# Performance work log

Hardware: AMD Instinct MI355X
Metric: run time of the kernel (lower is better)

Reference implementation:

```python
import jax, jax.numpy as jnp
import numpy as np

B, S, D, H, F = 8, 1024, 1024, 16, 4096
DH = D // H  # 64
EPS = 1e-12


def _layer_norm(x, g, b):
    mu = jnp.mean(x, axis=-1, keepdims=True)
    var = jnp.mean(jnp.square(x - mu), axis=-1, keepdims=True)
    return (x - mu) / jnp.sqrt(var + EPS) * g + b


def setup_inputs() -> dict:
    key = jax.random.key(0)
    ks = jax.random.split(key, 16)
    sd = 0.02
    inp = {
        "x": jax.random.normal(ks[0], (B, S, D), dtype=jnp.float32),
        "attn_mask": jnp.ones((B, S), dtype=jnp.int32),
        # attention projections (torch Linear: W is [out, in])
        "Wq": jax.random.normal(ks[1], (D, D), dtype=jnp.float32) * sd,
        "bq": jnp.zeros((D,), dtype=jnp.float32),
        "Wk": jax.random.normal(ks[2], (D, D), dtype=jnp.float32) * sd,
        "bk": jnp.zeros((D,), dtype=jnp.float32),
        "Wv": jax.random.normal(ks[3], (D, D), dtype=jnp.float32) * sd,
        "bv": jnp.zeros((D,), dtype=jnp.float32),
        "Wo": jax.random.normal(ks[4], (D, D), dtype=jnp.float32) * sd,
        "bo": jnp.zeros((D,), dtype=jnp.float32),
        # sa_layer_norm
        "ln1_g": jnp.ones((D,), dtype=jnp.float32),
        "ln1_b": jnp.zeros((D,), dtype=jnp.float32),
        # FFN
        "W1": jax.random.normal(ks[5], (F, D), dtype=jnp.float32) * sd,
        "b1": jnp.zeros((F,), dtype=jnp.float32),
        "W2": jax.random.normal(ks[6], (D, F), dtype=jnp.float32) * sd,
        "b2": jnp.zeros((D,), dtype=jnp.float32),
        # output_layer_norm
        "ln2_g": jnp.ones((D,), dtype=jnp.float32),
        "ln2_b": jnp.zeros((D,), dtype=jnp.float32),
    }
    return inp


def reference(x, attn_mask, Wq, bq, Wk, bk, Wv, bv, Wo, bo,
              ln1_g, ln1_b, W1, b1, W2, b2, ln2_g, ln2_b):
    b, s, d = x.shape

    def proj_heads(inp, W, bias):
        y = jnp.einsum('bsd,ed->bse', inp, W) + bias  # torch Linear: x @ W.T + b
        return y.reshape(b, s, H, DH).transpose(0, 2, 1, 3)  # (b, h, s, dh)

    q = proj_heads(x, Wq, bq) / jnp.sqrt(jnp.float32(DH))
    k = proj_heads(x, Wk, bk)
    v = proj_heads(x, Wv, bv)

    scores = jnp.einsum('bhqe,bhke->bhqk', q, k)  # (b, h, s, s)
    pad = (attn_mask == 0)[:, None, None, :]      # (b, 1, 1, s)
    scores = jnp.where(pad, -jnp.inf, scores)
    weights = jax.nn.softmax(scores, axis=-1)

    ctx = jnp.einsum('bhqk,bhke->bhqe', weights, v)
    ctx = ctx.transpose(0, 2, 1, 3).reshape(b, s, d)
    sa_out = jnp.einsum('bsd,ed->bse', ctx, Wo) + bo

    h = _layer_norm(sa_out + x, ln1_g, ln1_b)

    ff = jnp.einsum('bsd,fd->bsf', h, W1) + b1
    ff = jax.nn.gelu(ff, approximate=False)
    ff = jnp.einsum('bsf,df->bsd', ff, W2) + b2

    out = _layer_norm(ff + h, ln2_g, ln2_b)
    return out
```

## Files before the change

### kernel.cpp

```cpp
#include <hip/hip_runtime.h>
#include <math.h>

typedef __attribute__((ext_vector_type(8))) short short8;
typedef __attribute__((ext_vector_type(4))) float f32x4;

__device__ __forceinline__ unsigned short f2bf(float f) {
  unsigned int u = __float_as_uint(f);
  u += 0x7fffu + ((u >> 16) & 1u);
  return (unsigned short)(u >> 16);
}

__device__ __forceinline__ float gelu_f(float v) {
  float xa = fabsf(v) * 0.70710678118f;
  float t = __builtin_amdgcn_rcpf(1.f + 0.3275911f * xa);
  float p = t * (0.254829592f +
            t * (-0.284496736f +
            t * (1.421413741f +
            t * (-1.453152027f + t * 1.061405429f))));
  float erfa = 1.f - p * __expf(-xa * xa);
  return 0.5f * v * (1.f + copysignf(erfa, v));
}

__device__ __forceinline__ void gll16(const unsigned short* g, unsigned short* l) {
  __builtin_amdgcn_global_load_lds(
      (const __attribute__((address_space(1))) unsigned int*)(uintptr_t)g,
      (__attribute__((address_space(3))) unsigned int*)(uintptr_t)l, 16, 0, 0);
}

__global__ __launch_bounds__(256) void cvt_all(
    const float* __restrict__ Wq, const float* __restrict__ Wk,
    const float* __restrict__ Wv, const float* __restrict__ Wo,
    const float* __restrict__ W1, const float* __restrict__ W2,
    const float* __restrict__ x, unsigned short* __restrict__ ws) {
  const int bi = blockIdx.x;
  const float* in;
  unsigned short* out;
  int i;
  if (bi < 4096) {
    const int m = bi >> 10;
    in = (m == 0) ? Wq : (m == 1) ? Wk : (m == 2) ? Wv : Wo;
    out = ws + (size_t)m * (1u << 20);
    i = (bi & 1023) * 256 + threadIdx.x;
  } else if (bi < 8192) {
    in = W1; out = ws + (4u << 20); i = (bi - 4096) * 256 + threadIdx.x;
  } else if (bi < 12288) {
    in = W2; out = ws + (8u << 20); i = (bi - 8192) * 256 + threadIdx.x;
  } else {
    in = x; out = ws + (12u << 20); i = (bi - 12288) * 256 + threadIdx.x;
  }
  float4 f = reinterpret_cast<const float4*>(in)[i];
  ushort4 o;
  o.x = f2bf(f.x); o.y = f2bf(f.y); o.z = f2bf(f.z); o.w = f2bf(f.w);
  reinterpret_cast<ushort4*>(out)[i] = o;
}

template <int EPI, bool SWAP>
__global__ __launch_bounds__(256) void gemm_nt(
    const unsigned short* __restrict__ A, const unsigned short* __restrict__ B,
    const float* __restrict__ bias, const float* __restrict__ bias_k,
    int K, int N, const float* __restrict__ resid,
    unsigned short* __restrict__ outb, float* __restrict__ outf) {
  __shared__ __align__(16) unsigned short As[2][128 * 32];
  __shared__ __align__(16) unsigned short Bs[2][128 * 32];
  const int t = threadIdx.x;
  const int tm = blockIdx.y * 128, tn = blockIdx.x * 128;
  const int lane = t & 63, wv = t >> 6;
  const int wr = wv >> 1, wc = wv & 1;
  const int l15 = lane & 15, quad = lane >> 4;
  const int srow = lane >> 2;
  const int scol = (lane & 3) << 3;

  const unsigned short* pa0 = &A[(size_t)(tm + wv * 32 + srow) * K + scol];
  const unsigned short* pa1 = &A[(size_t)(tm + wv * 32 + 16 + srow) * K + scol];
  const unsigned short* pb0 = &B[(size_t)(tn + wv * 32 + srow) * K + scol];
  const unsigned short* pb1 = &B[(size_t)(tn + wv * 32 + 16 + srow) * K + scol];
  unsigned short* la0 = &As[0][(wv * 2) * 512];
  unsigned short* la1 = &As[0][(wv * 2 + 1) * 512];
  unsigned short* lb0 = &Bs[0][(wv * 2) * 512];
  unsigned short* lb1 = &Bs[0][(wv * 2 + 1) * 512];

  const f32x4 zero = {0.f, 0.f, 0.f, 0.f};
  f32x4 acc[4][4];
#pragma unroll
  for (int i = 0; i < 4; ++i)
#pragma unroll
    for (int j = 0; j < 4; ++j) acc[i][j] = zero;

  gll16(pa0, la0); pa0 += 32;
  gll16(pa1, la1); pa1 += 32;
  gll16(pb0, lb0); pb0 += 32;
  gll16(pb1, lb1); pb1 += 32;

  const int nIter = K >> 5;
  for (int it = 0; it < nIter; ++it) {
    __syncthreads();
    const int cur = (it & 1) * 4096;
    const int nxt = 4096 - cur;
    if (it + 1 < nIter) {
      gll16(pa0, la0 + nxt); pa0 += 32;
      gll16(pa1, la1 + nxt); pa1 += 32;
      gll16(pb0, lb0 + nxt); pb0 += 32;
      gll16(pb1, lb1 + nxt); pb1 += 32;
    }
    short8 af[4], bfr[4];
#pragma unroll
    for (int i = 0; i < 4; ++i) {
      af[i] = *reinterpret_cast<const short8*>(&As[0][cur + (wr * 64 + i * 16 + l15) * 32 + quad * 8]);
      bfr[i] = *reinterpret_cast<const short8*>(&Bs[0][cur + (wc * 64 + i * 16 + l15) * 32 + quad * 8]);
    }
#pragma unroll
    for (int i = 0; i < 4; ++i)
#pragma unroll
      for (int j = 0; j < 4; ++j)
        acc[i][j] = SWAP
            ? __builtin_amdgcn_mfma_f32_16x16x32_bf16(bfr[j], af[i], acc[i][j], 0, 0, 0)
            : __builtin_amdgcn_mfma_f32_16x16x32_bf16(af[i], bfr[j], acc[i][j], 0, 0, 0);
  }

  if (SWAP) {
#pragma unroll
    for (int i = 0; i < 4; ++i) {
      const int row = tm + wr * 64 + i * 16 + l15;
#pragma unroll
      for (int j = 0; j < 4; ++j) {
        const int col0 = tn + wc * 64 + j * 16 + quad * 4;
        if (EPI == 2) {
          const float4 b4 = *reinterpret_cast<const float4*>(&bias[col0]);
          ushort4 pk;
          pk.x = f2bf(gelu_f(acc[i][j][0] + b4.x));
          pk.y = f2bf(gelu_f(acc[i][j][1] + b4.y));
          pk.z = f2bf(gelu_f(acc[i][j][2] + b4.z));
          pk.w = f2bf(gelu_f(acc[i][j][3] + b4.w));
          *reinterpret_cast<ushort4*>(&outb[(size_t)row * (size_t)N + col0]) = pk;
        } else {
          const float4 b4 = *reinterpret_cast<const float4*>(&bias[col0]);
          const size_t idx = (size_t)row * (size_t)N + col0;
          const float4 r4 = *reinterpret_cast<const float4*>(&resid[idx]);
          float4 o4;
          o4.x = acc[i][j][0] + b4.x + r4.x;
          o4.y = acc[i][j][1] + b4.y + r4.y;
          o4.z = acc[i][j][2] + b4.z + r4.z;
          o4.w = acc[i][j][3] + b4.w + r4.w;
          *reinterpret_cast<float4*>(&outf[idx]) = o4;
        }
      }
    }
  } else {
#pragma unroll
    for (int i = 0; i < 4; ++i) {
#pragma unroll
      for (int j = 0; j < 4; ++j) {
        const int col = tn + wc * 64 + j * 16 + l15;
        const float bcol = bias[col];
        const int h = col >> 6, dh = col & 63;
        const int row0 = tm + wr * 64 + i * 16 + quad * 4;
        const int b = row0 >> 10, s0 = row0 & 1023;
        ushort4 pk;
        pk.x = f2bf(acc[i][j][0] + bcol);
        pk.y = f2bf(acc[i][j][1] + bcol);
        pk.z = f2bf(acc[i][j][2] + bcol);
        pk.w = f2bf(acc[i][j][3] + bcol);
        *reinterpret_cast<ushort4*>(
            &outb[(((size_t)((b << 4) + h)) << 16) + (dh << 10) + s0]) = pk;
      }
    }
  }
}

#define MFMA_Q(mh, nh)                                                        \
  {                                                                           \
    __builtin_amdgcn_s_setprio(1);                                            \
    _Pragma("unroll") for (int i = 0; i < 4; ++i) {                           \
      _Pragma("unroll") for (int jj = 0; jj < NREP / 2; ++jj) {               \
        const int j = (nh) * (NREP / 2) + jj;                                 \
        acc[(mh) * 4 + i][j] = __builtin_amdgcn_mfma_f32_16x16x32_bf16(       \
            bf[j][0], af[i][0], acc[(mh) * 4 + i][j], 0, 0, 0);               \
        acc[(mh) * 4 + i][j] = __builtin_amdgcn_mfma_f32_16x16x32_bf16(       \
            bf[j][1], af[i][1], acc[(mh) * 4 + i][j], 0, 0, 0);               \
      }                                                                       \
    }                                                                         \
    __builtin_amdgcn_s_setprio(0);                                            \
  }

#define READ_A(mh)                                                            \
  _Pragma("unroll") for (int i = 0; i < 4; ++i) {                             \
    af[i][0] = *reinterpret_cast<const short8*>(                              \
        &Asc[abase + ((mh) * 64 + i * 16) * 64 + s0]);                        \
    af[i][1] = *reinterpret_cast<const short8*>(                              \
        &Asc[abase + ((mh) * 64 + i * 16) * 64 + s1]);                        \
  }

#define LGKM0                                                                 \
  asm volatile("s_waitcnt lgkmcnt(0)" ::: "memory");                          \
  __builtin_amdgcn_sched_barrier(0)

#define MEMFENCE asm volatile("" ::: "memory")

template <int EPI, int BN>
__global__ __launch_bounds__(512, 2) void gemm_big(
    const unsigned short* __restrict__ A, const unsigned short* __restrict__ B,
    const float* __restrict__ bias, const float* __restrict__ bias_k,
    int K, int N, const float* __restrict__ resid,
    unsigned short* __restrict__ outb, float* __restrict__ outf) {
  constexpr int WN = BN / 4;
  constexpr int NREP = WN / 16;
  constexpr int BGRP = BN / 64;
  __shared__ __align__(16) unsigned short As[2][256 * 64];
  __shared__ __align__(16) unsigned short Bs[2][BN * 64];

  const int t = threadIdx.x;
  const int lane = t & 63, wv = t >> 6;
  const int wm = wv >> 2, wn = wv & 3;
  const int l15 = lane & 15, quad = lane >> 4;

  const int gx = gridDim.x;
  const int nwg = gx * gridDim.y;
  int lin = blockIdx.y * gx + blockIdx.x;
  lin = (lin & 7) * (nwg >> 3) + (lin >> 3);
  const int gxs = 31 - __clz(gx);
  const int tn = (lin & (gx - 1)) * BN;
  const int tm = (lin >> gxs) * 256;

  const int srow = lane >> 3;
  const int scol = ((lane & 7) ^ srow) << 3;
  const unsigned short* pA[4];
  const unsigned short* pB[BGRP];
#pragma unroll
  for (int g = 0; g < 4; ++g)
    pA[g] = &A[(size_t)(tm + g * 64 + wv * 8 + srow) * K + scol];
#pragma unroll
  for (int g = 0; g < BGRP; ++g)
    pB[g] = &B[(size_t)(tn + g * 64 + wv * 8 + srow) * K + scol];

  const int abase = (wm * 128 + l15) * 64;
  const int bbase = (wn * WN + l15) * 64;
  const int s0 = ((quad ^ (l15 & 7)) << 3);
  const int s1 = (((quad + 4) ^ (l15 & 7)) << 3);

  const f32x4 zero = {0.f, 0.f, 0.f, 0.f};
  f32x4 acc[8][NREP];
#pragma unroll
  for (int i = 0; i < 8; ++i)
#pragma unroll
    for (int j = 0; j < NREP; ++j) acc[i][j] = zero;
  short8 af[4][2], bf[NREP][2];

#pragma unroll
  for (int g = 0; g < 4; ++g) gll16(pA[g], &As[0][(g * 64 + wv * 8) * 64]);
#pragma unroll
  for (int g = 0; g < BGRP; ++g) gll16(pB[g], &Bs[0][(g * 64 + wv * 8) * 64]);
#pragma unroll
  for (int g = 0; g < 4; ++g) {
    pA[g] += 64;
    gll16(pA[g], &As[1][(g * 64 + wv * 8) * 64]);
    pA[g] += 64;
  }
#pragma unroll
  for (int g = 0; g < BGRP; ++g) {
    pB[g] += 64;
    gll16(pB[g], &Bs[1][(g * 64 + wv * 8) * 64]);
    pB[g] += 64;
  }
  if constexpr (BGRP == 4) asm volatile("s_waitcnt vmcnt(8)" ::: "memory");
  else asm volatile("s_waitcnt vmcnt(6)" ::: "memory");
  __builtin_amdgcn_s_barrier();
  MEMFENCE;

  const int NT = K >> 6;
  for (int tt = 0; tt < NT; ++tt) {
    const unsigned short* Asc = As[tt & 1];
    const unsigned short* Bsc = Bs[tt & 1];
    unsigned short* Asw = As[tt & 1];
    unsigned short* Bsw = Bs[tt & 1];
    const bool st = (tt + 2 < NT);

    READ_A(0);
#pragma unroll
    for (int j = 0; j < NREP; ++j) {
      bf[j][0] = *reinterpret_cast<const short8*>(&Bsc[bbase + (j * 16) * 64 + s0]);
      bf[j][1] = *reinterpret_cast<const short8*>(&Bsc[bbase + (j * 16) * 64 + s1]);
    }
    LGKM0;
    MFMA_Q(0, 0);
    MFMA_Q(0, 1);
    __builtin_amdgcn_s_barrier();
    MEMFENCE;
    if (st) {
      gll16(pA[0], &Asw[(0 * 64 + wv * 8) * 64]);
      gll16(pA[2], &Asw[(2 * 64 + wv * 8) * 64]);
      gll16(pB[0], &Bsw[(0 * 64 + wv * 8) * 64]);
      if constexpr (BGRP == 4) gll16(pB[1], &Bsw[(1 * 64 + wv * 8) * 64]);
    }
    READ_A(1);
    LGKM0;
    MFMA_Q(1, 0);
    __builtin_amdgcn_s_barrier();
    MEMFENCE;
    if (st) {
      gll16(pA[1], &Asw[(1 * 64 + wv * 8) * 64]);
      gll16(pA[3], &Asw[(3 * 64 + wv * 8) * 64]);
      if constexpr (BGRP == 4) {
        gll16(pB[2], &Bsw[(2 * 64 + wv * 8) * 64]);
        gll16(pB[3], &Bsw[(3 * 64 + wv * 8) * 64]);
      } else {
        gll16(pB[1], &Bsw[(1 * 64 + wv * 8) * 64]);
      }
#pragma unroll
      for (int g = 0; g < 4; ++g) pA[g] += 64;
#pragma unroll
      for (int g = 0; g < BGRP; ++g) pB[g] += 64;
    }
    MFMA_Q(1, 1);
    if (st) {
      if constexpr (BGRP == 4) asm volatile("s_waitcnt vmcnt(8)" ::: "memory");
      else asm volatile("s_waitcnt vmcnt(6)" ::: "memory");
    } else {
      asm volatile("s_waitcnt vmcnt(0)" ::: "memory");
    }
    __builtin_amdgcn_s_barrier();
    MEMFENCE;
  }

  const int rb = tm + wm * 128 + l15;
  const int cb = tn + wn * WN + (quad << 2);
#pragma unroll
  for (int i = 0; i < 8; ++i) {
    const int row = rb + i * 16;
#pragma unroll
    for (int j = 0; j < NREP; ++j) {
      const int col0 = cb + j * 16;
      if constexpr (EPI == 5) {
        const int chunk = col0 >> 10;
        const int colc = col0 & 1023;
        const float4 b4 = *reinterpret_cast<const float4*>(
            &(chunk == 0 ? bias : bias_k)[colc]);
        const float sc = (chunk == 0) ? 0.125f : 1.f;
        const int h = colc >> 6, dh = colc & 63;
        const int b = row >> 10, s = row & 1023;
        ushort4 pk;
        pk.x = f2bf((acc[i][j][0] + b4.x) * sc);
        pk.y = f2bf((acc[i][j][1] + b4.y) * sc);
        pk.z = f2bf((acc[i][j][2] + b4.z) * sc);
        pk.w = f2bf((acc[i][j][3] + b4.w) * sc);
        *reinterpret_cast<ushort4*>(
            &outb[((size_t)chunk << 23) + (((size_t)((b << 4) + h)) << 16) +
                  (s << 6) + dh]) = pk;
      } else if constexpr (EPI == 2) {
        const float4 b4 = *reinterpret_cast<const float4*>(&bias[col0]);
        ushort4 pk;
        pk.x = f2bf(gelu_f(acc[i][j][0] + b4.x));
        pk.y = f2bf(gelu_f(acc[i][j][1] + b4.y));
        pk.z = f2bf(gelu_f(acc[i][j][2] + b4.z));
        pk.w = f2bf(gelu_f(acc[i][j][3] + b4.w));
        *reinterpret_cast<ushort4*>(&outb[(size_t)row * (size_t)N + col0]) = pk;
      } else {
        const float4 b4 = *reinterpret_cast<const float4*>(&bias[col0]);
        const size_t idx = (size_t)row * (size_t)N + col0;
        const float4 r4 = *reinterpret_cast<const float4*>(&resid[idx]);
        float4 o4;
        o4.x = acc[i][j][0] + b4.x + r4.x;
        o4.y = acc[i][j][1] + b4.y + r4.y;
        o4.z = acc[i][j][2] + b4.z + r4.z;
        o4.w = acc[i][j][3] + b4.w + r4.w;
        *reinterpret_cast<float4*>(&outf[idx]) = o4;
      }
    }
  }
}
#undef MFMA_Q
#undef READ_A
#undef LGKM0
#undef MEMFENCE

__global__ __launch_bounds__(256) void attn_kernel(
    const unsigned short* __restrict__ Q, const unsigned short* __restrict__ Kc,
    const unsigned short* __restrict__ Vg, const int* __restrict__ mask,
    unsigned short* __restrict__ ctx) {
  __shared__ __align__(16) unsigned short Ks[2][64 * 64];
  __shared__ __align__(16) unsigned short Vs[2][64 * 64];
  __shared__ __align__(16) unsigned short Ps[4][16 * 72];
  __shared__ float maskf[1024];
  const int t = threadIdx.x;
  const int bh = blockIdx.x;
  const int qt = blockIdx.y;
  const int b = bh >> 4, h = bh & 15;
  const int lane = t & 63, wv = t >> 6, l15 = lane & 15, quad = lane >> 4;
  const int lr = lane >> 3;
  const int cs = (lane & 7) ^ lr;
  const unsigned short* Qp = Q + ((size_t)bh << 16);
  const unsigned short* Kp = Kc + ((size_t)bh << 16);
  const unsigned short* Vp = Vg + ((size_t)bh << 16);
  const int seg0 = wv * 2, seg1 = wv * 2 + 1;
  const int r0 = seg0 * 8 + lr, r1 = seg1 * 8 + lr;

  for (int i = t; i < 1024; i += 256)
    maskf[i] = mask[b * 1024 + i] ? -8.f : -INFINITY;

  short8 qf[2][2];
#pragma unroll
  for (int g = 0; g < 2; ++g)
#pragma unroll
    for (int hh = 0; hh < 2; ++hh)
      qf[g][hh] = *reinterpret_cast<const short8*>(
          &Qp[(size_t)(qt * 128 + wv * 32 + g * 16 + l15) * 64 + hh * 32 + quad * 8]);

  gll16(&Kp[r0 * 64 + cs * 8], &Ks[0][seg0 * 512]);
  gll16(&Kp[r1 * 64 + cs * 8], &Ks[0][seg1 * 512]);
  gll16(&Vp[r0 * 1024 + cs * 8], &Vs[0][seg0 * 512]);
  gll16(&Vp[r1 * 1024 + cs * 8], &Vs[0][seg1 * 512]);

  const int sw0 = ((quad ^ (l15 & 7)) << 3);
  const int sw1 = (((quad + 4) ^ (l15 & 7)) << 3);
  const f32x4 zero = {0.f, 0.f, 0.f, 0.f};
  float ps[2][4];
  f32x4 o[2][4];
#pragma unroll
  for (int g = 0; g < 2; ++g)
#pragma unroll
    for (int j = 0; j < 4; ++j) { o[g][j] = zero; ps[g][j] = 0.f; }

  unsigned short* Pw = Ps[wv];
  for (int kt = 0; kt < 16; ++kt) {
    __syncthreads();
    const int cur = kt & 1;
    if (kt < 15) {
      const int nb = cur ^ 1;
      gll16(&Kp[((kt + 1) * 64 + r0) * 64 + cs * 8], &Ks[nb][seg0 * 512]);
      gll16(&Kp[((kt + 1) * 64 + r1) * 64 + cs * 8], &Ks[nb][seg1 * 512]);
      gll16(&Vp[r0 * 1024 + (kt + 1) * 64 + cs * 8], &Vs[nb][seg0 * 512]);
      gll16(&Vp[r1 * 1024 + (kt + 1) * 64 + cs * 8], &Vs[nb][seg1 * 512]);
    }
    float madd[4];
    short8 kf[4][2];
#pragma unroll
    for (int nt = 0; nt < 4; ++nt) {
      const int row = (nt * 16 + l15) * 64;
      kf[nt][0] = *reinterpret_cast<const short8*>(&Ks[cur][row + sw0]);
      kf[nt][1] = *reinterpret_cast<const short8*>(&Ks[cur][row + sw1]);
      madd[nt] = maskf[kt * 64 + nt * 16 + l15];
    }
#pragma unroll
    for (int g = 0; g < 2; ++g) {
      f32x4 s4[4];
#pragma unroll
      for (int nt = 0; nt < 4; ++nt) {
        s4[nt] = __builtin_amdgcn_mfma_f32_16x16x32_bf16(qf[g][0], kf[nt][0], zero, 0, 0, 0);
        s4[nt] = __builtin_amdgcn_mfma_f32_16x16x32_bf16(qf[g][1], kf[nt][1], s4[nt], 0, 0, 0);
      }
#pragma unroll
      for (int nt = 0; nt < 4; ++nt) {
#pragma unroll
        for (int r = 0; r < 4; ++r) {
          float p = __expf(s4[nt][r] + madd[nt]);
          ps[g][r] += p;
          Pw[(quad * 4 + r) * 72 + nt * 16 + l15] = f2bf(p);
        }
      }
      short8 pf0 = *reinterpret_cast<const short8*>(&Pw[l15 * 72 + quad * 8]);
      short8 pf1 = *reinterpret_cast<const short8*>(&Pw[l15 * 72 + 32 + quad * 8]);
#pragma unroll
      for (int nt = 0; nt < 4; ++nt) {
        const int row = (nt * 16 + l15) * 64;
        short8 vf0 = *reinterpret_cast<const short8*>(&Vs[cur][row + sw0]);
        short8 vf1 = *reinterpret_cast<const short8*>(&Vs[cur][row + sw1]);
        o[g][nt] = __builtin_amdgcn_mfma_f32_16x16x32_bf16(pf0, vf0, o[g][nt], 0, 0, 0);
        o[g][nt] = __builtin_amdgcn_mfma_f32_16x16x32_bf16(pf1, vf1, o[g][nt], 0, 0, 0);
      }
    }
  }

#pragma unroll
  for (int g = 0; g < 2; ++g)
#pragma unroll
    for (int r = 0; r < 4; ++r) {
      float v = ps[g][r];
#pragma unroll
      for (int off = 8; off >= 1; off >>= 1) v += __shfl_xor(v, off, 64);
      const float inv = 1.f / v;
      const int srow = qt * 128 + wv * 32 + g * 16 + quad * 4 + r;
#pragma unroll
      for (int nt = 0; nt < 4; ++nt) {
        const int dh = nt * 16 + l15;
        ctx[((size_t)b << 20) + ((size_t)srow << 10) + (h << 6) + dh] =
            f2bf(o[g][nt][r] * inv);
      }
    }
}

__global__ __launch_bounds__(256) void ln_kernel(float* __restrict__ y,
                                                 const float* __restrict__ g,
                                                 const float* __restrict__ be,
                                                 unsigned short* __restrict__ hb) {
  __shared__ float sm[8];
  const int t = threadIdx.x;
  const size_t row = blockIdx.x;
  float* yr = y + (row << 10);
  float v[4];
#pragma unroll
  for (int i = 0; i < 4; ++i) v[i] = yr[t + (i << 8)];
  float s = v[0] + v[1] + v[2] + v[3];
#pragma unroll
  for (int off = 32; off >= 1; off >>= 1) s += __shfl_xor(s, off, 64);
  if ((t & 63) == 0) sm[t >> 6] = s;
  __syncthreads();
  float mu = (sm[0] + sm[1] + sm[2] + sm[3]) * (1.f / 1024.f);
  float q = 0.f;
#pragma unroll
  for (int i = 0; i < 4; ++i) { float d = v[i] - mu; q += d * d; }
#pragma unroll
  for (int off = 32; off >= 1; off >>= 1) q += __shfl_xor(q, off, 64);
  if ((t & 63) == 0) sm[4 + (t >> 6)] = q;
  __syncthreads();
  float var = (sm[4] + sm[5] + sm[6] + sm[7]) * (1.f / 1024.f);
  float rs = rsqrtf(var + 1e-12f);
#pragma unroll
  for (int i = 0; i < 4; ++i) {
    int c = t + (i << 8);
    float o = (v[i] - mu) * rs * g[c] + be[c];
    yr[c] = o;
    if (hb) hb[(row << 10) + c] = f2bf(o);
  }
}

extern "C" void kernel_launch(void* const* d_in, const int* in_sizes, int n_in,
                              void* d_out, int out_size, void* d_ws, size_t ws_size,
                              hipStream_t stream) {
  const float* x   = (const float*)d_in[0];
  const int*   msk = (const int*)d_in[1];
  const float* Wq  = (const float*)d_in[2];
  const float* bq  = (const float*)d_in[3];
  const float* Wk  = (const float*)d_in[4];
  const float* bk  = (const float*)d_in[5];
  const float* Wv  = (const float*)d_in[6];
  const float* bv  = (const float*)d_in[7];
  const float* Wo  = (const float*)d_in[8];
  const float* bo  = (const float*)d_in[9];
  const float* g1  = (const float*)d_in[10];
  const float* be1 = (const float*)d_in[11];
  const float* W1  = (const float*)d_in[12];
  const float* b1  = (const float*)d_in[13];
  const float* W2  = (const float*)d_in[14];
  const float* b2  = (const float*)d_in[15];
  const float* g2  = (const float*)d_in[16];
  const float* be2 = (const float*)d_in[17];
  float* out = (float*)d_out;

  unsigned short* Wqb = (unsigned short*)d_ws;
  unsigned short* Wvb = Wqb + (2u << 20);
  unsigned short* Wob = Wvb + (1u << 20);
  unsigned short* W1b = Wob + (1u << 20);
  unsigned short* W2b = W1b + (4u << 20);
  unsigned short* xb  = W2b + (4u << 20);
  unsigned short* qb  = xb + (8u << 20);
  unsigned short* vb  = qb + (16u << 20);
  unsigned short* ctx = xb;
  unsigned short* ffb = xb;
  float* y1 = (float*)(qb + (24u << 20));
  unsigned short* hb = (unsigned short*)(y1 + (8u << 20));

  dim3 blk(256), blk5(512);
  cvt_all<<<dim3(20480), blk, 0, stream>>>(Wq, Wk, Wv, Wo, W1, W2, x, (unsigned short*)d_ws);
  gemm_big<5, 256><<<dim3(8, 32), blk5, 0, stream>>>(xb, Wqb, bq, bk, 1024, 2048,
                                                     nullptr, qb, nullptr);
  gemm_nt<4, false><<<dim3(8, 64), blk, 0, stream>>>(xb, Wvb, bv, nullptr, 1024, 1024,
                                                     nullptr, vb, nullptr);
  attn_kernel<<<dim3(128, 8), blk, 0, stream>>>(qb, qb + (8u << 20), vb, msk, ctx);
  gemm_big<1, 128><<<dim3(8, 32), blk5, 0, stream>>>(ctx, Wob, bo, nullptr, 1024, 1024,
                                                     x, nullptr, y1);
  ln_kernel<<<dim3(8192), blk, 0, stream>>>(y1, g1, be1, hb);
  gemm_big<2, 256><<<dim3(16, 32), blk5, 0, stream>>>(hb, W1b, b1, nullptr, 1024, 4096,
                                                      nullptr, ffb, nullptr);
  gemm_big<1, 128><<<dim3(8, 32), blk5, 0, stream>>>(ffb, W2b, b2, nullptr, 4096, 1024,
                                                     y1, nullptr, out);
  ln_kernel<<<dim3(8192), blk, 0, stream>>>(out, g2, be2, nullptr);
}
```

Baseline: 501.5 us.

## Unify V projection into gemm_big and restructure its LDS/MFMA interleave schedule

Removes the older 128x128 gemm_nt kernel and routes the V projection through gemm_big with a new SWAP template flag that handles the transposed V output layout. The main loop of gemm_big is reorganised into four quarter phases, each with its own LDS read, barrier, MFMA block and staggered global-to-LDS prefetch. The aim is to overlap LDS fragment reads and global loads more finely with MFMA work. It adds more barriers per iteration, which could cost extra synchronisation.

```diff
diff --git a/kernel.cpp b/kernel.cpp
--- a/kernel.cpp
+++ b/kernel.cpp
@@ -54,77 +54,229 @@
   reinterpret_cast<ushort4*>(out)[i] = o;
 }
 
-template <int EPI, bool SWAP>
-__global__ __launch_bounds__(256) void gemm_nt(
+#define MFMA_Q(mh, nh)                                                        \
+  {                                                                           \
+    __builtin_amdgcn_s_setprio(1);                                            \
+    _Pragma("unroll") for (int i = 0; i < 4; ++i) {                           \
+      _Pragma("unroll") for (int jj = 0; jj < NREP / 2; ++jj) {               \
+        const int j = (nh) * (NREP / 2) + jj;                                 \
+        if constexpr (SWAP) {                                                 \
+          acc[(mh) * 4 + i][j] = __builtin_amdgcn_mfma_f32_16x16x32_bf16(     \
+              bf[j][0], af[i][0], acc[(mh) * 4 + i][j], 0, 0, 0);             \
+          acc[(mh) * 4 + i][j] = __builtin_amdgcn_mfma_f32_16x16x32_bf16(     \
+              bf[j][1], af[i][1], acc[(mh) * 4 + i][j], 0, 0, 0);             \
+        } else {                                                              \
+          acc[(mh) * 4 + i][j] = __builtin_amdgcn_mfma_f32_16x16x32_bf16(     \
+              af[i][0], bf[j][0], acc[(mh) * 4 + i][j], 0, 0, 0);             \
+          acc[(mh) * 4 + i][j] = __builtin_amdgcn_mfma_f32_16x16x32_bf16(     \
+              af[i][1], bf[j][1], acc[(mh) * 4 + i][j], 0, 0, 0);             \
+        }                                                                     \
+      }                                                                       \
+    }                                                                         \
+    __builtin_amdgcn_s_setprio(0);                                            \
+  }
+
+#define READ_A(mh)                                                            \
+  _Pragma("unroll") for (int i = 0; i < 4; ++i) {                             \
+    af[i][0] = *reinterpret_cast<const short8*>(                              \
+        &Asc[abase + ((mh) * 64 + i * 16) * 64 + s0]);                        \
+    af[i][1] = *reinterpret_cast<const short8*>(                              \
+        &Asc[abase + ((mh) * 64 + i * 16) * 64 + s1]);                        \
+  }
+
+#define READ_B(nh)                                                            \
+  _Pragma("unroll") for (int jj = 0; jj < NREP / 2; ++jj) {                   \
+    const int j = (nh) * (NREP / 2) + jj;                                     \
+    bf[j][0] = *reinterpret_cast<const short8*>(                              \
+        &Bsc[bbase + (j * 16) * 64 + s0]);                                    \
+    bf[j][1] = *reinterpret_cast<const short8*>(                              \
+        &Bsc[bbase + (j * 16) * 64 + s1]);                                    \
+  }
+
+#define LGKM0                                                                 \
+  asm volatile("s_waitcnt lgkmcnt(0)" ::: "memory");                          \
+  __builtin_amdgcn_sched_barrier(0)
+
+#define MEMFENCE asm volatile("" ::: "memory")
+#define BAR __builtin_amdgcn_s_barrier()
+
+template <int EPI, int BN, bool SWAP>
+__global__ __launch_bounds__(512, 2) void gemm_big(
     const unsigned short* __restrict__ A, const unsigned short* __restrict__ B,
     const float* __restrict__ bias, const float* __restrict__ bias_k,
     int K, int N, const float* __restrict__ resid,
     unsigned short* __restrict__ outb, float* __restrict__ outf) {
-  __shared__ __align__(16) unsigned short As[2][128 * 32];
-  __shared__ __align__(16) unsigned short Bs[2][128 * 32];
+  constexpr int WN = BN / 4;
+  constexpr int NREP = WN / 16;
+  constexpr int BGRP = BN / 64;
+  __shared__ __align__(16) unsigned short As[2][256 * 64];
+  __shared__ __align__(16) unsigned short Bs[2][BN * 64];
+
   const int t = threadIdx.x;
-  const int tm = blockIdx.y * 128, tn = blockIdx.x * 128;
   const int lane = t & 63, wv = t >> 6;
-  const int wr = wv >> 1, wc = wv & 1;
+  const int wm = wv >> 2, wn = wv & 3;
   const int l15 = lane & 15, quad = lane >> 4;
-  const int srow = lane >> 2;
-  const int scol = (lane & 3) << 3;
-
-  const unsigned short* pa0 = &A[(size_t)(tm + wv * 32 + srow) * K + scol];
-  const unsigned short* pa1 = &A[(size_t)(tm + wv * 32 + 16 + srow) * K + scol];
-  const unsigned short* pb0 = &B[(size_t)(tn + wv * 32 + srow) * K + scol];
-  const unsigned short* pb1 = &B[(size_t)(tn + wv * 32 + 16 + srow) * K + scol];
-  unsigned short* la0 = &As[0][(wv * 2) * 512];
-  unsigned short* la1 = &As[0][(wv * 2 + 1) * 512];
-  unsigned short* lb0 = &Bs[0][(wv * 2) * 512];
-  unsigned short* lb1 = &Bs[0][(wv * 2 + 1) * 512];
+
+  const int gx = gridDim.x;
+  const int nwg = gx * gridDim.y;
+  int lin = blockIdx.y * gx + blockIdx.x;
+  lin = (lin & 7) * (nwg >> 3) + (lin >> 3);
+  const int gxs = 31 - __clz(gx);
+  const int tn = (lin & (gx - 1)) * BN;
+  const int tm = (lin >> gxs) * 256;
+
+  const int srow = lane >> 3;
+  const int scol = ((lane & 7) ^ srow) << 3;
+  const unsigned short* pA[4];
+  const unsigned short* pB[BGRP];
+#pragma unroll
+  for (int g = 0; g < 4; ++g)
+    pA[g] = &A[(size_t)(tm + g * 64 + wv * 8 + srow) * K + scol];
+#pragma unroll
+  for (int g = 0; g < BGRP; ++g)
+    pB[g] = &B[(size_t)(tn + g * 64 + wv * 8 + srow) * K + scol];
+
+  const int abase = (wm * 128 + l15) * 64;
+  const int bbase = (wn * WN + l15) * 64;
+  const int s0 = ((quad ^ (l15 & 7)) << 3);
+  const int s1 = (((quad + 4) ^ (l15 & 7)) << 3);
 
   const f32x4 zero = {0.f, 0.f, 0.f, 0.f};
-  f32x4 acc[4][4];
-#pragma unroll
-  for (int i = 0; i < 4; ++i)
-#pragma unroll
-    for (int j = 0; j < 4; ++j) acc[i][j] = zero;
-
-  gll16(pa0, la0); pa0 += 32;
-  gll16(pa1, la1); pa1 += 32;
-  gll16(pb0, lb0); pb0 += 32;
-  gll16(pb1, lb1); pb1 += 32;
-
-  const int nIter = K >> 5;
-  for (int it = 0; it < nIter; ++it) {
-    __syncthreads();
-    const int cur = (it & 1) * 4096;
-    const int nxt = 4096 - cur;
-    if (it + 1 < nIter) {
-      gll16(pa0, la0 + nxt); pa0 += 32;
-      gll16(pa1, la1 + nxt); pa1 += 32;
-      gll16(pb0, lb0 + nxt); pb0 += 32;
-      gll16(pb1, lb1 + nxt); pb1 += 32;
-    }
-    short8 af[4], bfr[4];
-#pragma unroll
-    for (int i = 0; i < 4; ++i) {
-      af[i] = *reinterpret_cast<const short8*>(&As[0][cur + (wr * 64 + i * 16 + l15) * 32 + quad * 8]);
-      bfr[i] = *reinterpret_cast<const short8*>(&Bs[0][cur + (wc * 64 + i * 16 + l15) * 32 + quad * 8]);
-    }
-#pragma unroll
-    for (int i = 0; i < 4; ++i)
-#pragma unroll
-      for (int j = 0; j < 4; ++j)
-        acc[i][j] = SWAP
-            ? __builtin_amdgcn_mfma_f32_16x16x32_bf16(bfr[j], af[i], acc[i][j], 0, 0, 0)
-            : __builtin_amdgcn_mfma_f32_16x16x32_bf16(af[i], bfr[j], acc[i][j], 0, 0, 0);
-  }
-
-  if (SWAP) {
-#pragma unroll
-    for (int i = 0; i < 4; ++i) {
-      const int row = tm + wr * 64 + i * 16 + l15;
-#pragma unroll
-      for (int j = 0; j < 4; ++j) {
-        const int col0 = tn + wc * 64 + j * 16 + quad * 4;
-        if (EPI == 2) {
+  f32x4 acc[8][NREP];
+#pragma unroll
+  for (int i = 0; i < 8; ++i)
+#pragma unroll
+    for (int j = 0; j < NREP; ++j) acc[i][j] = zero;
+  short8 af[4][2], bf[NREP][2];
+
+#pragma unroll
+  for (int g = 0; g < 4; ++g) gll16(pA[g], &As[0][(g * 64 + wv * 8) * 64]);
+#pragma unroll
+  for (int g = 0; g < BGRP; ++g) gll16(pB[g], &Bs[0][(g * 64 + wv * 8) * 64]);
+#pragma unroll
+  for (int g = 0; g < 4; ++g) {
+    pA[g] += 64;
+    gll16(pA[g], &As[1][(g * 64 + wv * 8) * 64]);
+    pA[g] += 64;
+  }
+#pragma unroll
+  for (int g = 0; g < BGRP; ++g) {
+    pB[g] += 64;
+    gll16(pB[g], &Bs[1][(g * 64 + wv * 8) * 64]);
+    pB[g] += 64;
+  }
+  if constexpr (BGRP == 4) asm volatile("s_waitcnt vmcnt(8)" ::: "memory");
+  else asm volatile("s_waitcnt vmcnt(6)" ::: "memory");
+  BAR;
+  MEMFENCE;
+
+  const int NT = K >> 6;
+  for (int tt = 0; tt < NT; ++tt) {
+    const unsigned short* Asc = As[tt & 1];
+    const unsigned short* Bsc = Bs[tt & 1];
+    unsigned short* Asw = As[tt & 1];
+    unsigned short* Bsw = Bs[tt & 1];
+    const bool st = (tt + 2 < NT);
+
+    READ_A(0);
+    READ_B(0);
+    asm volatile("s_waitcnt lgkmcnt(8)" ::: "memory");
+    MEMFENCE; BAR;
+    LGKM0;
+    MFMA_Q(0, 0);
+    MEMFENCE; BAR;
+
+    READ_B(1);
+    if (st) {
+      gll16(pA[0], &Asw[(0 * 64 + wv * 8) * 64]);
+      gll16(pA[2], &Asw[(2 * 64 + wv * 8) * 64]);
+    }
+    MEMFENCE; BAR;
+    LGKM0;
+    MFMA_Q(0, 1);
+    MEMFENCE; BAR;
+
+    READ_A(1);
+    if (st) {
+      gll16(pB[0], &Bsw[(0 * 64 + wv * 8) * 64]);
+      if constexpr (BGRP == 4) gll16(pB[1], &Bsw[(1 * 64 + wv * 8) * 64]);
+    }
+    MEMFENCE; BAR;
+    LGKM0;
+    MFMA_Q(1, 0);
+    MEMFENCE; BAR;
+
+    if (st) {
+      gll16(pA[1], &Asw[(1 * 64 + wv * 8) * 64]);
+      gll16(pA[3], &Asw[(3 * 64 + wv * 8) * 64]);
+      if constexpr (BGRP == 4) {
+        gll16(pB[2], &Bsw[(2 * 64 + wv * 8) * 64]);
+        gll16(pB[3], &Bsw[(3 * 64 + wv * 8) * 64]);
+      } else {
+        gll16(pB[1], &Bsw[(1 * 64 + wv * 8) * 64]);
+      }
+#pragma unroll
+      for (int g = 0; g < 4; ++g) pA[g] += 64;
+#pragma unroll
+      for (int g = 0; g < BGRP; ++g) pB[g] += 64;
+    }
+    MFMA_Q(1, 1);
+    if (st) {
+      if constexpr (BGRP == 4) asm volatile("s_waitcnt vmcnt(8)" ::: "memory");
+      else asm volatile("s_waitcnt vmcnt(6)" ::: "memory");
+    } else {
+      asm volatile("s_waitcnt vmcnt(0)" ::: "memory");
+    }
+    MEMFENCE; BAR;
+  }
+
+  if constexpr (!SWAP) {
+    const int rb2 = tm + wm * 128 + (quad << 2);
+    const int cb2 = tn + wn * WN + l15;
+#pragma unroll
+    for (int i = 0; i < 8; ++i) {
+      const int row0 = rb2 + i * 16;
+#pragma unroll
+      for (int j = 0; j < NREP; ++j) {
+        const int col = cb2 + j * 16;
+        const float bcol = bias[col];
+        const int h = col >> 6, dh = col & 63;
+        const int b = row0 >> 10, s0r = row0 & 1023;
+        ushort4 pk;
+        pk.x = f2bf(acc[i][j][0] + bcol);
+        pk.y = f2bf(acc[i][j][1] + bcol);
+        pk.z = f2bf(acc[i][j][2] + bcol);
+        pk.w = f2bf(acc[i][j][3] + bcol);
+        *reinterpret_cast<ushort4*>(
+            &outb[(((size_t)((b << 4) + h)) << 16) + (dh << 10) + s0r]) = pk;
+      }
+    }
+  } else {
+    const int rb = tm + wm * 128 + l15;
+    const int cb = tn + wn * WN + (quad << 2);
+#pragma unroll
+    for (int i = 0; i < 8; ++i) {
+      const int row = rb + i * 16;
+#pragma unroll
+      for (int j = 0; j < NREP; ++j) {
+        const int col0 = cb + j * 16;
+        if constexpr (EPI == 5) {
+          const int chunk = col0 >> 10;
+          const int colc = col0 & 1023;
+          const float4 b4 = *reinterpret_cast<const float4*>(
+              &(chunk == 0 ? bias : bias_k)[colc]);
+          const float sc = (chunk == 0) ? 0.125f : 1.f;
+          const int h = colc >> 6, dh = colc & 63;
+          const int b = row >> 10, s = row & 1023;
+          ushort4 pk;
+          pk.x = f2bf((acc[i][j][0] + b4.x) * sc);
+          pk.y = f2bf((acc[i][j][1] + b4.y) * sc);
+          pk.z = f2bf((acc[i][j][2] + b4.z) * sc);
+          pk.w = f2bf((acc[i][j][3] + b4.w) * sc);
+          *reinterpret_cast<ushort4*>(
+              &outb[((size_t)chunk << 23) + (((size_t)((b << 4) + h)) << 16) +
+                    (s << 6) + dh]) = pk;
+        } else if constexpr (EPI == 2) {
           const float4 b4 = *reinterpret_cast<const float4*>(&bias[col0]);
           ushort4 pk;
           pk.x = f2bf(gelu_f(acc[i][j][0] + b4.x));
@@ -145,232 +297,14 @@
         }
       }
     }
-  } else {
-#pragma unroll
-    for (int i = 0; i < 4; ++i) {
-#pragma unroll
-      for (int j = 0; j < 4; ++j) {
-        const int col = tn + wc * 64 + j * 16 + l15;
-        const float bcol = bias[col];
-        const int h = col >> 6, dh = col & 63;
-        const int row0 = tm + wr * 64 + i * 16 + quad * 4;
-        const int b = row0 >> 10, s0 = row0 & 1023;
-        ushort4 pk;
-        pk.x = f2bf(acc[i][j][0] + bcol);
-        pk.y = f2bf(acc[i][j][1] + bcol);
-        pk.z = f2bf(acc[i][j][2] + bcol);
-        pk.w = f2bf(acc[i][j][3] + bcol);
-        *reinterpret_cast<ushort4*>(
-            &outb[(((size_t)((b << 4) + h)) << 16) + (dh << 10) + s0]) = pk;
-      }
-    }
-  }
-}
-
-#define MFMA_Q(mh, nh)                                                        \
-  {                                                                           \
-    __builtin_amdgcn_s_setprio(1);                                            \
-    _Pragma("unroll") for (int i = 0; i < 4; ++i) {                           \
-      _Pragma("unroll") for (int jj = 0; jj < NREP / 2; ++jj) {               \
-        const int j = (nh) * (NREP / 2) + jj;                                 \
-        acc[(mh) * 4 + i][j] = __builtin_amdgcn_mfma_f32_16x16x32_bf16(       \
-            bf[j][0], af[i][0], acc[(mh) * 4 + i][j], 0, 0, 0);               \
-        acc[(mh) * 4 + i][j] = __builtin_amdgcn_mfma_f32_16x16x32_bf16(       \
-            bf[j][1], af[i][1], acc[(mh) * 4 + i][j], 0, 0, 0);               \
-      }                                                                       \
-    }                                                                         \
-    __builtin_amdgcn_s_setprio(0);                                            \
-  }
-
-#define READ_A(mh)                                                            \
-  _Pragma("unroll") for (int i = 0; i < 4; ++i) {                             \
-    af[i][0] = *reinterpret_cast<const short8*>(                              \
-        &Asc[abase + ((mh) * 64 + i * 16) * 64 + s0]);                        \
-    af[i][1] = *reinterpret_cast<const short8*>(                              \
-        &Asc[abase + ((mh) * 64 + i * 16) * 64 + s1]);                        \
-  }
-
-#define LGKM0                                                                 \
-  asm volatile("s_waitcnt lgkmcnt(0)" ::: "memory");                          \
-  __builtin_amdgcn_sched_barrier(0)
-
-#define MEMFENCE asm volatile("" ::: "memory")
-
-template <int EPI, int BN>
-__global__ __launch_bounds__(512, 2) void gemm_big(
-    const unsigned short* __restrict__ A, const unsigned short* __restrict__ B,
-    const float* __restrict__ bias, const float* __restrict__ bias_k,
-    int K, int N, const float* __restrict__ resid,
-    unsigned short* __restrict__ outb, float* __restrict__ outf) {
-  constexpr int WN = BN / 4;
-  constexpr int NREP = WN / 16;
-  constexpr int BGRP = BN / 64;
-  __shared__ __align__(16) unsigned short As[2][256 * 64];
-  __shared__ __align__(16) unsigned short Bs[2][BN * 64];
-
-  const int t = threadIdx.x;
-  const int lane = t & 63, wv = t >> 6;
-  const int wm = wv >> 2, wn = wv & 3;
-  const int l15 = lane & 15, quad = lane >> 4;
-
-  const int gx = gridDim.x;
-  const int nwg = gx * gridDim.y;
-  int lin = blockIdx.y * gx + blockIdx.x;
-  lin = (lin & 7) * (nwg >> 3) + (lin >> 3);
-  const int gxs = 31 - __clz(gx);
-  const int tn = (lin & (gx - 1)) * BN;
-  const int tm = (lin >> gxs) * 256;
-
-  const int srow = lane >> 3;
-  const int scol = ((lane & 7) ^ srow) << 3;
-  const unsigned short* pA[4];
-  const unsigned short* pB[BGRP];
-#pragma unroll
-  for (int g = 0; g < 4; ++g)
-    pA[g] = &A[(size_t)(tm + g * 64 + wv * 8 + srow) * K + scol];
-#pragma unroll
-  for (int g = 0; g < BGRP; ++g)
-    pB[g] = &B[(size_t)(tn + g * 64 + wv * 8 + srow) * K + scol];
-
-  const int abase = (wm * 128 + l15) * 64;
-  const int bbase = (wn * WN + l15) * 64;
-  const int s0 = ((quad ^ (l15 & 7)) << 3);
-  const int s1 = (((quad + 4) ^ (l15 & 7)) << 3);
-
-  const f32x4 zero = {0.f, 0.f, 0.f, 0.f};
-  f32x4 acc[8][NREP];
-#pragma unroll
-  for (int i = 0; i < 8; ++i)
-#pragma unroll
-    for (int j = 0; j < NREP; ++j) acc[i][j] = zero;
-  short8 af[4][2], bf[NREP][2];
-
-#pragma unroll
-  for (int g = 0; g < 4; ++g) gll16(pA[g], &As[0][(g * 64 + wv * 8) * 64]);
-#pragma unroll
-  for (int g = 0; g < BGRP; ++g) gll16(pB[g], &Bs[0][(g * 64 + wv * 8) * 64]);
-#pragma unroll
-  for (int g = 0; g < 4; ++g) {
-    pA[g] += 64;
-    gll16(pA[g], &As[1][(g * 64 + wv * 8) * 64]);
-    pA[g] += 64;
-  }
-#pragma unroll
-  for (int g = 0; g < BGRP; ++g) {
-    pB[g] += 64;
-    gll16(pB[g], &Bs[1][(g * 64 + wv * 8) * 64]);
-    pB[g] += 64;
-  }
-  if constexpr (BGRP == 4) asm volatile("s_waitcnt vmcnt(8)" ::: "memory");
-  else asm volatile("s_waitcnt vmcnt(6)" ::: "memory");
-  __builtin_amdgcn_s_barrier();
-  MEMFENCE;
-
-  const int NT = K >> 6;
-  for (int tt = 0; tt < NT; ++tt) {
-    const unsigned short* Asc = As[tt & 1];
-    const unsigned short* Bsc = Bs[tt & 1];
-    unsigned short* Asw = As[tt & 1];
-    unsigned short* Bsw = Bs[tt & 1];
-    const bool st = (tt + 2 < NT);
-
-    READ_A(0);
-#pragma unroll
-    for (int j = 0; j < NREP; ++j) {
-      bf[j][0] = *reinterpret_cast<const short8*>(&Bsc[bbase + (j * 16) * 64 + s0]);
-      bf[j][1] = *reinterpret_cast<const short8*>(&Bsc[bbase + (j * 16) * 64 + s1]);
-    }
-    LGKM0;
-    MFMA_Q(0, 0);
-    MFMA_Q(0, 1);
-    __builtin_amdgcn_s_barrier();
-    MEMFENCE;
-    if (st) {
-      gll16(pA[0], &Asw[(0 * 64 + wv * 8) * 64]);
-      gll16(pA[2], &Asw[(2 * 64 + wv * 8) * 64]);
-      gll16(pB[0], &Bsw[(0 * 64 + wv * 8) * 64]);
-      if constexpr (BGRP == 4) gll16(pB[1], &Bsw[(1 * 64 + wv * 8) * 64]);
-    }
-    READ_A(1);
-    LGKM0;
-    MFMA_Q(1, 0);
-    __builtin_amdgcn_s_barrier();
-    MEMFENCE;
-    if (st) {
-      gll16(pA[1], &Asw[(1 * 64 + wv * 8) * 64]);
-      gll16(pA[3], &Asw[(3 * 64 + wv * 8) * 64]);
-      if constexpr (BGRP == 4) {
-        gll16(pB[2], &Bsw[(2 * 64 + wv * 8) * 64]);
-        gll16(pB[3], &Bsw[(3 * 64 + wv * 8) * 64]);
-      } else {
-        gll16(pB[1], &Bsw[(1 * 64 + wv * 8) * 64]);
-      }
-#pragma unroll
-      for (int g = 0; g < 4; ++g) pA[g] += 64;
-#pragma unroll
-      for (int g = 0; g < BGRP; ++g) pB[g] += 64;
-    }
-    MFMA_Q(1, 1);
-    if (st) {
-      if constexpr (BGRP == 4) asm volatile("s_waitcnt vmcnt(8)" ::: "memory");
-      else asm volatile("s_waitcnt vmcnt(6)" ::: "memory");
-    } else {
-      asm volatile("s_waitcnt vmcnt(0)" ::: "memory");
-    }
-    __builtin_amdgcn_s_barrier();
-    MEMFENCE;
-  }
-
-  const int rb = tm + wm * 128 + l15;
-  const int cb = tn + wn * WN + (quad << 2);
-#pragma unroll
-  for (int i = 0; i < 8; ++i) {
-    const int row = rb + i * 16;
-#pragma unroll
-    for (int j = 0; j < NREP; ++j) {
-      const int col0 = cb + j * 16;
-      if constexpr (EPI == 5) {
-        const int chunk = col0 >> 10;
-        const int colc = col0 & 1023;
-        const float4 b4 = *reinterpret_cast<const float4*>(
-            &(chunk == 0 ? bias : bias_k)[colc]);
-        const float sc = (chunk == 0) ? 0.125f : 1.f;
-        const int h = colc >> 6, dh = colc & 63;
-        const int b = row >> 10, s = row & 1023;
-        ushort4 pk;
-        pk.x = f2bf((acc[i][j][0] + b4.x) * sc);
-        pk.y = f2bf((acc[i][j][1] + b4.y) * sc);
-        pk.z = f2bf((acc[i][j][2] + b4.z) * sc);
-        pk.w = f2bf((acc[i][j][3] + b4.w) * sc);
-        *reinterpret_cast<ushort4*>(
-            &outb[((size_t)chunk << 23) + (((size_t)((b << 4) + h)) << 16) +
-                  (s << 6) + dh]) = pk;
-      } else if constexpr (EPI == 2) {
-        const float4 b4 = *reinterpret_cast<const float4*>(&bias[col0]);
-        ushort4 pk;
-        pk.x = f2bf(gelu_f(acc[i][j][0] + b4.x));
-        pk.y = f2bf(gelu_f(acc[i][j][1] + b4.y));
-        pk.z = f2bf(gelu_f(acc[i][j][2] + b4.z));
-        pk.w = f2bf(gelu_f(acc[i][j][3] + b4.w));
-        *reinterpret_cast<ushort4*>(&outb[(size_t)row * (size_t)N + col0]) = pk;
-      } else {
-        const float4 b4 = *reinterpret_cast<const float4*>(&bias[col0]);
-        const size_t idx = (size_t)row * (size_t)N + col0;
-        const float4 r4 = *reinterpret_cast<const float4*>(&resid[idx]);
-        float4 o4;
-        o4.x = acc[i][j][0] + b4.x + r4.x;
-        o4.y = acc[i][j][1] + b4.y + r4.y;
-        o4.z = acc[i][j][2] + b4.z + r4.z;
-        o4.w = acc[i][j][3] + b4.w + r4.w;
-        *reinterpret_cast<float4*>(&outf[idx]) = o4;
-      }
-    }
   }
 }
 #undef MFMA_Q
 #undef READ_A
+#undef READ_B
 #undef LGKM0
 #undef MEMFENCE
+#undef BAR
 
 __global__ __launch_bounds__(256) void attn_kernel(
     const unsigned short* __restrict__ Q, const unsigned short* __restrict__ Kc,
@@ -560,17 +494,17 @@
 
   dim3 blk(256), blk5(512);
   cvt_all<<<dim3(20480), blk, 0, stream>>>(Wq, Wk, Wv, Wo, W1, W2, x, (unsigned short*)d_ws);
-  gemm_big<5, 256><<<dim3(8, 32), blk5, 0, stream>>>(xb, Wqb, bq, bk, 1024, 2048,
-                                                     nullptr, qb, nullptr);
-  gemm_nt<4, false><<<dim3(8, 64), blk, 0, stream>>>(xb, Wvb, bv, nullptr, 1024, 1024,
-                                                     nullptr, vb, nullptr);
+  gemm_big<5, 256, true><<<dim3(8, 32), blk5, 0, stream>>>(xb, Wqb, bq, bk, 1024, 2048,
+                                                           nullptr, qb, nullptr);
+  gemm_big<4, 128, false><<<dim3(8, 32), blk5, 0, stream>>>(xb, Wvb, bv, nullptr, 1024, 1024,
+                                                            nullptr, vb, nullptr);
   attn_kernel<<<dim3(128, 8), blk, 0, stream>>>(qb, qb + (8u << 20), vb, msk, ctx);
-  gemm_big<1, 128><<<dim3(8, 32), blk5, 0, stream>>>(ctx, Wob, bo, nullptr, 1024, 1024,
-                                                     x, nullptr, y1);
+  gemm_big<1, 128, true><<<dim3(8, 32), blk5, 0, stream>>>(ctx, Wob, bo, nullptr, 1024, 1024,
+                                                           x, nullptr, y1);
   ln_kernel<<<dim3(8192), blk, 0, stream>>>(y1, g1, be1, hb);
-  gemm_big<2, 256><<<dim3(16, 32), blk5, 0, stream>>>(hb, W1b, b1, nullptr, 1024, 4096,
-                                                      nullptr, ffb, nullptr);
-  gemm_big<1, 128><<<dim3(8, 32), blk5, 0, stream>>>(ffb, W2b, b2, nullptr, 4096, 1024,
-                                                     y1, nullptr, out);
+  gemm_big<2, 256, true><<<dim3(16, 32), blk5, 0, stream>>>(hb, W1b, b1, nullptr, 1024, 4096,
+                                                            nullptr, ffb, nullptr);
+  gemm_big<1, 128, true><<<dim3(8, 32), blk5, 0, stream>>>(ffb, W2b, b2, nullptr, 4096, 1024,
+                                                           y1, nullptr, out);
   ln_kernel<<<dim3(8192), blk, 0, stream>>>(out, g2, be2, nullptr);
 }
```

Result: no change. 503.1 us (+0.3%).
